# Performance work log

Measured on AMD Instinct MI355X. Metric: run time of the kernel, lower is better.

Reference implementation:

```python
import jax, jax.numpy as jnp
import numpy as np

N, E, G = 50000, 500000, 64
F_IN, H, C = 10, 4, 64
HC = H * C  # 256
NCLS = 8
BN_EPS = 1e-5


def _bn(x, g, b, m, v):
    # eval-mode BatchNorm1d with running stats
    return (x - m) * jax.lax.rsqrt(v + BN_EPS) * g + b


def _gat(x, src, dst, W, a_s, a_d, b):
    # PyG GATConv (concat=True): h=[N,H,C]; e_ij=leakyrelu(a_s.h_j + a_d.h_i);
    # softmax over incoming edges of each destination node; scatter-add.
    n = x.shape[0]
    h = (x @ W).reshape(n, H, C)
    es = jnp.einsum('nhc,hc->nh', h, a_s)  # source term per node
    ed = jnp.einsum('nhc,hc->nh', h, a_d)  # dest term per node
    e = jax.nn.leaky_relu(es[src] + ed[dst], 0.2)            # [E2,H]
    m = jax.ops.segment_max(e, dst, num_segments=n)
    ex = jnp.exp(e - m[dst])
    s = jax.ops.segment_sum(ex, dst, num_segments=n)
    alpha = ex / (s[dst] + 1e-16)                             # [E2,H]
    out = jax.ops.segment_sum(h[src] * alpha[:, :, None], dst, num_segments=n)
    return out.reshape(n, HC) + b, alpha


def _gcn(x, src, dst, W, b):
    n = x.shape[0]
    deg = jax.ops.segment_sum(jnp.ones_like(src, dtype=x.dtype), dst, num_segments=n)
    dinv = jax.lax.rsqrt(jnp.maximum(deg, 1.0))
    norm = dinv[src] * dinv[dst]
    xw = x @ W
    return jax.ops.segment_sum(xw[src] * norm[:, None], dst, num_segments=n) + b


def setup_inputs() -> dict:
    key = jax.random.key(0)
    ks = jax.random.split(key, 48)
    r = lambda i, sh, sc=0.1: jax.random.normal(ks[i], sh, dtype=jnp.float32) * sc
    p = {}
    p['x'] = jax.random.normal(ks[0], (N, F_IN), dtype=jnp.float32)
    p['edge_index'] = jax.random.randint(ks[1], (2, E), 0, N, dtype=jnp.int32)
    p['batch'] = jnp.sort(jax.random.randint(ks[2], (N,), 0, G, dtype=jnp.int32))
    # GAT1
    p['W1'] = r(3, (F_IN, HC)); p['as1'] = r(4, (H, C)); p['ad1'] = r(5, (H, C)); p['bi1'] = r(6, (HC,))
    # GAT2
    p['W2'] = r(7, (HC, HC)); p['as2'] = r(8, (H, C)); p['ad2'] = r(9, (H, C)); p['bi2'] = r(10, (HC,))
    # BN running stats / affine
    for i, (nm, d) in enumerate([('bn1', HC), ('bn2', HC), ('bn3', C)]):
        k0 = 11 + 4 * i
        p[nm + '_g'] = 1.0 + r(k0, (d,))
        p[nm + '_b'] = r(k0 + 1, (d,))
        p[nm + '_m'] = r(k0 + 2, (d,))
        p[nm + '_v'] = 1.0 + jax.random.uniform(ks[k0 + 3], (d,), dtype=jnp.float32) * 0.5
    # GCN
    p['Wg'] = r(23, (HC, C)); p['bg'] = r(24, (C,))
    # reduce_dim
    p['Wr'] = r(25, (2 * C, C)); p['br'] = r(26, (C,))
    # rul head
    p['Wh1'] = r(27, (C, 32)); p['bh1'] = r(28, (32,))
    p['Wh2'] = r(29, (32, 16)); p['bh2'] = r(30, (16,))
    p['Wh3'] = r(31, (16, 1)); p['bh3'] = r(32, (1,))
    # location head
    p['Wl1'] = r(33, (C, 32)); p['bl1'] = r(34, (32,))
    p['Wl2'] = r(35, (32, NCLS)); p['bl2'] = r(36, (NCLS,))
    # energy head
    p['We1'] = r(37, (C, 16)); p['be1'] = r(38, (16,))
    p['We2'] = r(39, (16, 1)); p['be2'] = r(40, (1,))
    return p


def reference(x, edge_index, batch,
              W1, as1, ad1, bi1, W2, as2, ad2, bi2,
              bn1_g, bn1_b, bn1_m, bn1_v, bn2_g, bn2_b, bn2_m, bn2_v,
              bn3_g, bn3_b, bn3_m, bn3_v,
              Wg, bg, Wr, br,
              Wh1, bh1, Wh2, bh2, Wh3, bh3,
              Wl1, bl1, Wl2, bl2, We1, be1, We2, be2):
    n = x.shape[0]
    loop = jnp.arange(n, dtype=edge_index.dtype)
    src = jnp.concatenate([edge_index[0], loop])
    dst = jnp.concatenate([edge_index[1], loop])

    h, alpha1 = _gat(x, src, dst, W1, as1, ad1, bi1)
    h = jax.nn.elu(_bn(h, bn1_g, bn1_b, bn1_m, bn1_v))  # dropout = identity (eval)
    h, alpha2 = _gat(h, src, dst, W2, as2, ad2, bi2)
    h = jax.nn.elu(_bn(h, bn2_g, bn2_b, bn2_m, bn2_v))
    h = _gcn(h, src, dst, Wg, bg)
    h = jax.nn.elu(_bn(h, bn3_g, bn3_b, bn3_m, bn3_v))  # node embeddings [N,64]

    cnt = jax.ops.segment_sum(jnp.ones((n,), h.dtype), batch, num_segments=G)
    x_mean = jax.ops.segment_sum(h, batch, num_segments=G) / jnp.maximum(cnt, 1.0)[:, None]
    x_max = jax.ops.segment_max(h, batch, num_segments=G)
    x_max = jnp.where(cnt[:, None] > 0, x_max, 0.0)
    xg = jnp.concatenate([x_mean, x_max], axis=1) @ Wr + br  # [G,64]

    t = jax.nn.relu(xg @ Wh1 + bh1)
    t = jax.nn.relu(t @ Wh2 + bh2)
    rul = jax.nn.sigmoid(t @ Wh3 + bh3) * 100.0
    loc = jax.nn.relu(xg @ Wl1 + bl1) @ Wl2 + bl2
    en = jax.nn.relu(xg @ We1 + be1) @ We2 + be2
    return rul, loc, en, h, xg
```

## Files before the change

kernel.cpp:

```cpp
#include <hip/hip_runtime.h>
#include <math.h>

#define SCAN_BLK 1024
#define BN_EPS 1e-5f

typedef __attribute__((ext_vector_type(8))) short short8;
typedef __attribute__((ext_vector_type(4))) short short4v;
typedef __attribute__((ext_vector_type(4))) float f32x4;

__device__ __forceinline__ float eluf(float x){ return x > 0.f ? x : (expf(x) - 1.f); }
__device__ __forceinline__ unsigned short f2bf(float f){
  unsigned u = __float_as_uint(f);
  u += 0x7FFFu + ((u >> 16) & 1u);
  return (unsigned short)(u >> 16);
}
__device__ __forceinline__ float bf2f(unsigned short s){
  return __uint_as_float(((unsigned)s) << 16);
}
__device__ __forceinline__ unsigned fmap(float f){
  unsigned b = __float_as_uint(f);
  return (b & 0x80000000u) ? ~b : (b | 0x80000000u);
}
__device__ __forceinline__ float funmap(unsigned u){
  unsigned b = (u & 0x80000000u) ? (u ^ 0x80000000u) : ~u;
  return __uint_as_float(b);
}
__device__ __forceinline__ float lrelu(float a){ return a > 0.f ? a : 0.2f * a; }

__global__ void k_count(const int* __restrict__ ei, int* __restrict__ deg, int ne, int e2)
{
  int t = blockIdx.x * 256 + threadIdx.x;
  if (t >= e2) return;
  int dst = (t < ne) ? ei[ne + t] : t - ne;
  atomicAdd(&deg[dst], 1);
}

__global__ void k_scan1(const int* __restrict__ deg, int* __restrict__ rowptr,
                        int* __restrict__ partials, int n)
{
  __shared__ int sh[SCAN_BLK];
  int t = threadIdx.x, base = blockIdx.x * SCAN_BLK;
  int v = (base + t < n) ? deg[base + t] : 0;
  sh[t] = v;
  __syncthreads();
  for (int off = 1; off < SCAN_BLK; off <<= 1) {
    int u = 0;
    if (t >= off) u = sh[t - off];
    __syncthreads();
    if (t >= off) sh[t] += u;
    __syncthreads();
  }
  if (base + t < n) rowptr[base + t] = sh[t] - v;
  if (t == SCAN_BLK - 1) partials[blockIdx.x] = sh[t];
}

__global__ void k_scan2(int* __restrict__ rowptr, const int* __restrict__ partials, int n)
{
  int base = blockIdx.x * SCAN_BLK;
  int add = 0;
  for (int i = 0; i < blockIdx.x; i++) add += partials[i];
  int t = threadIdx.x;
  if (base + t < n) rowptr[base + t] += add;
}

__global__ void k_fill(const int* __restrict__ ei, const int* __restrict__ rowptr,
                       int* __restrict__ cursor, int* __restrict__ col, int ne, int e2)
{
  int t = blockIdx.x * 256 + threadIdx.x;
  if (t >= e2) return;
  int src, dst;
  if (t < ne) { src = ei[t]; dst = ei[ne + t]; } else { src = dst = t - ne; }
  int pos = rowptr[dst] + atomicAdd(&cursor[dst], 1);
  col[pos] = src;
}

__global__ void k_dinv(const int* __restrict__ deg, float* __restrict__ dinv, int n)
{
  int t = blockIdx.x * 256 + threadIdx.x;
  if (t < n) dinv[t] = rsqrtf(fmaxf((float)deg[t], 1.f));
}

__global__ void k_pack(const float* __restrict__ W, unsigned short* __restrict__ Wp,
                       int N, int nct)
{
  int tid = threadIdx.x;
  int l = tid >> 3, j = tid & 7;
  int ct = blockIdx.x >> 3, ks = blockIdx.x & 7;
  int k = ks * 32 + (l >> 4) * 8 + j;
  int c = ct * 16 + (l & 15);
  Wp[(size_t)(ks * nct + ct) * 512 + tid] = f2bf(W[(size_t)k * N + c]);
}

__global__ void k_pack_es(const float* __restrict__ WasT, unsigned short* __restrict__ Wes)
{
  int tid = threadIdx.x;
  int l = tid >> 3, j = tid & 7;
  int ks = blockIdx.x;
  int k = ks * 32 + (l >> 4) * 8 + j;
  int c = l & 15;
  float v = (c < 8) ? WasT[(size_t)c * 256 + k] : 0.f;
  Wes[(size_t)(ks * 64 + l) * 8 + j] = f2bf(v);
}

__global__ void k_prep1(const float* __restrict__ W1, const float* __restrict__ as1,
                        const float* __restrict__ ad1,
                        float* __restrict__ Ws1, float* __restrict__ Wd1)
{
  int t = threadIdx.x;
  if (t >= 80) return;
  int half = t / 40, r = t % 40;
  int k = r / 4, h = r % 4;
  const float* a = half ? ad1 : as1;
  float s = 0.f;
  for (int c = 0; c < 64; c++) s += W1[k * 256 + h * 64 + c] * a[h * 64 + c];
  (half ? Wd1 : Ws1)[k * 4 + h] = s;
}

__global__ void k_prep2(const float* __restrict__ W2, const float* __restrict__ as2,
                        const float* __restrict__ ad2, float* __restrict__ WasT)
{
  int g = blockIdx.x * 256 + threadIdx.x;
  if (g >= 2048) return;
  int half = g >= 1024, r = g & 1023;
  int i = r >> 2, h = r & 3;
  const float* a = half ? ad2 : as2;
  float s = 0.f;
  for (int c = 0; c < 64; c++) s += W2[(size_t)i * 256 + h * 64 + c] * a[h * 64 + c];
  WasT[(size_t)(half * 4 + h) * 256 + i] = s;
}

__global__ void k_prep_bn(const float* __restrict__ bi1, const float* __restrict__ g1,
                          const float* __restrict__ b1, const float* __restrict__ m1,
                          const float* __restrict__ v1,
                          const float* __restrict__ bi2, const float* __restrict__ g2,
                          const float* __restrict__ b2, const float* __restrict__ m2,
                          const float* __restrict__ v2,
                          float* __restrict__ A1, float* __restrict__ B1,
                          float* __restrict__ A2, float* __restrict__ B2)
{
  int c = threadIdx.x;
  if (c < 256) {
    float a = rsqrtf(v1[c] + BN_EPS) * g1[c];
    A1[c] = a; B1[c] = (bi1[c] - m1[c]) * a + b1[c];
    a = rsqrtf(v2[c] + BN_EPS) * g2[c];
    A2[c] = a; B2[c] = (bi2[c] - m2[c]) * a + b2[c];
  }
}

__global__ void k_es1(const float* __restrict__ x, const float* __restrict__ Ws1,
                      const float* __restrict__ Wd1,
                      float* __restrict__ es, float* __restrict__ ed, int n)
{
  int t = blockIdx.x * 256 + threadIdx.x;
  if (t >= n) return;
  float xr[10];
  #pragma unroll
  for (int k = 0; k < 10; k++) xr[k] = x[(size_t)t * 10 + k];
  float e0[4] = {0,0,0,0}, e1[4] = {0,0,0,0};
  #pragma unroll
  for (int k = 0; k < 10; k++) {
    #pragma unroll
    for (int h = 0; h < 4; h++) {
      e0[h] += xr[k] * Ws1[k * 4 + h];
      e1[h] += xr[k] * Wd1[k * 4 + h];
    }
  }
  *(float4*)&es[t * 4] = make_float4(e0[0], e0[1], e0[2], e0[3]);
  *(float4*)&ed[t * 4] = make_float4(e1[0], e1[1], e1[2], e1[3]);
}

__global__ __launch_bounds__(256) void k_mfma_esed(
    const unsigned short* __restrict__ act, const unsigned short* __restrict__ Wes,
    float* __restrict__ es, float* __restrict__ ed, int n)
{
  int tid = threadIdx.x, wave = tid >> 6, lane = tid & 63;
  int l15 = lane & 15, lg = lane >> 4;
  int rbase = blockIdx.x * 64 + wave * 16;
  int arow = rbase + l15; if (arow > n - 1) arow = n - 1;
  const unsigned short* ap = &act[(size_t)arow * 256 + lg * 8];

  f32x4 acc = {0.f, 0.f, 0.f, 0.f};
  #pragma unroll
  for (int ks = 0; ks < 8; ks++) {
    short8 a = *(const short8*)(ap + ks * 32);
    short8 b = *(const short8*)&Wes[(size_t)(ks * 64 + lane) * 8];
    acc = __builtin_amdgcn_mfma_f32_16x16x32_bf16(a, b, acc, 0, 0, 0);
  }

  #pragma unroll
  for (int r = 0; r < 4; r++) {
    int row = rbase + lg * 4 + r;
    if (row < n) {
      if (l15 < 4)            es[row * 4 + l15] = acc[r];
      else if (l15 < 8)       ed[row * 4 + (l15 - 4)] = acc[r];
    }
  }
}

__global__ void k_xagg(const int* __restrict__ rowptr, const int* __restrict__ deg,
                       const int* __restrict__ col,
                       const float* __restrict__ es, const float* __restrict__ ed,
                       const float* __restrict__ x, float* __restrict__ xa, int n)
{
  int d = blockIdx.x * 4 + (threadIdx.x >> 6);
  if (d >= n) return;
  int lane = threadIdx.x & 63;
  int slot = lane >> 4, k = lane & 15;
  int start = rowptr[d], cnt = deg[d];
  bool active = (k < 10);
  float4 edv = *(const float4*)&ed[d * 4];

  float a0 = 0.f, a1 = 0.f, a2 = 0.f, a3 = 0.f;
  float s0 = 0.f, s1 = 0.f, s2 = 0.f, s3 = 0.f;
  int i = slot;
  for (; i + 4 < cnt; i += 8) {
    int e0 = start + i, e1 = start + i + 4;
    int sa = col[e0], sb = col[e1];
    float4 u0 = *(const float4*)&es[sa * 4];
    float4 u1 = *(const float4*)&es[sb * 4];
    float x0 = active ? x[(size_t)sa * 10 + k] : 0.f;
    float x1 = active ? x[(size_t)sb * 10 + k] : 0.f;
    float ex;
    ex = expf(lrelu(u0.x + edv.x)); a0 += ex * x0; s0 += ex;
    ex = expf(lrelu(u0.y + edv.y)); a1 += ex * x0; s1 += ex;
    ex = expf(lrelu(u0.z + edv.z)); a2 += ex * x0; s2 += ex;
    ex = expf(lrelu(u0.w + edv.w)); a3 += ex * x0; s3 += ex;
    ex = expf(lrelu(u1.x + edv.x)); a0 += ex * x1; s0 += ex;
    ex = expf(lrelu(u1.y + edv.y)); a1 += ex * x1; s1 += ex;
    ex = expf(lrelu(u1.z + edv.z)); a2 += ex * x1; s2 += ex;
    ex = expf(lrelu(u1.w + edv.w)); a3 += ex * x1; s3 += ex;
  }
  if (i < cnt) {
    int e0 = start + i;
    int sa = col[e0];
    float4 u0 = *(const float4*)&es[sa * 4];
    float x0 = active ? x[(size_t)sa * 10 + k] : 0.f;
    float ex;
    ex = expf(lrelu(u0.x + edv.x)); a0 += ex * x0; s0 += ex;
    ex = expf(lrelu(u0.y + edv.y)); a1 += ex * x0; s1 += ex;
    ex = expf(lrelu(u0.z + edv.z)); a2 += ex * x0; s2 += ex;
    ex = expf(lrelu(u0.w + edv.w)); a3 += ex * x0; s3 += ex;
  }
  a0 += __shfl_xor(a0, 16, 64); a0 += __shfl_xor(a0, 32, 64);
  a1 += __shfl_xor(a1, 16, 64); a1 += __shfl_xor(a1, 32, 64);
  a2 += __shfl_xor(a2, 16, 64); a2 += __shfl_xor(a2, 32, 64);
  a3 += __shfl_xor(a3, 16, 64); a3 += __shfl_xor(a3, 32, 64);
  s0 += __shfl_xor(s0, 16, 64); s0 += __shfl_xor(s0, 32, 64);
  s1 += __shfl_xor(s1, 16, 64); s1 += __shfl_xor(s1, 32, 64);
  s2 += __shfl_xor(s2, 16, 64); s2 += __shfl_xor(s2, 32, 64);
  s3 += __shfl_xor(s3, 16, 64); s3 += __shfl_xor(s3, 32, 64);

  if (slot == 0 && active) {
    float* xo = &xa[(size_t)d * 40];
    xo[k]      = a0 / (s0 + 1e-16f);
    xo[10 + k] = a1 / (s1 + 1e-16f);
    xo[20 + k] = a2 / (s2 + 1e-16f);
    xo[30 + k] = a3 / (s3 + 1e-16f);
  }
}

__global__ void k_gemm_xa(const float* __restrict__ xa, const float* __restrict__ W1,
                          const float* __restrict__ A1, const float* __restrict__ B1,
                          unsigned short* __restrict__ actA, int n)
{
  __shared__ float xal[160];
  int tid = threadIdx.x;
  int n0 = blockIdx.x * 4;
  if (tid < 160 && (size_t)n0 * 40 + tid < (size_t)n * 40)
    xal[tid] = xa[(size_t)n0 * 40 + tid];
  __syncthreads();
  int c = tid, h = c >> 6;
  float w[10];
  #pragma unroll
  for (int k = 0; k < 10; k++) w[k] = W1[k * 256 + c];
  float a1 = A1[c], b1 = B1[c];
  #pragma unroll
  for (int m = 0; m < 4; m++) {
    int nn = n0 + m;
    if (nn >= n) break;
    float acc = 0.f;
    #pragma unroll
    for (int k = 0; k < 10; k++) acc += xal[m * 40 + h * 10 + k] * w[k];
    actA[(size_t)nn * 256 + c] = f2bf(eluf(acc * a1 + b1));
  }
}

__global__ void k_gat_gather(const int* __restrict__ rowptr, const int* __restrict__ deg,
                             const int* __restrict__ col,
                             const float* __restrict__ es, const float* __restrict__ ed,
                             const unsigned short* __restrict__ act,
                             unsigned short* __restrict__ outb, int n)
{
  int d = blockIdx.x * 4 + (threadIdx.x >> 6);
  if (d >= n) return;
  int lane = threadIdx.x & 63;
  int half = lane >> 5, l32 = lane & 31;
  int c8 = l32 * 8, head = l32 >> 3;
  int start = rowptr[d], cnt = deg[d];
  float edh = ed[d * 4 + head];

  float acc[8] = {0.f,0.f,0.f,0.f,0.f,0.f,0.f,0.f};
  float sex = 0.f;
  int T = (cnt > half) ? ((cnt - half + 1) >> 1) : 0;
  int ebase = start + half;
  int t = 0;
  for (; t + 4 <= T; t += 4) {
    int e0 = ebase + 2 * t, e1 = e0 + 2, e2 = e0 + 4, e3 = e0 + 6;
    int s0 = col[e0], s1 = col[e1], s2 = col[e2], s3 = col[e3];
    float x0 = expf(lrelu(es[s0 * 4 + head] + edh));
    float x1 = expf(lrelu(es[s1 * 4 + head] + edh));
    float x2 = expf(lrelu(es[s2 * 4 + head] + edh));
    float x3 = expf(lrelu(es[s3 * 4 + head] + edh));
    short8 h0 = *(const short8*)&act[(size_t)s0 * 256 + c8];
    short8 h1 = *(const short8*)&act[(size_t)s1 * 256 + c8];
    short8 h2 = *(const short8*)&act[(size_t)s2 * 256 + c8];
    short8 h3 = *(const short8*)&act[(size_t)s3 * 256 + c8];
    #pragma unroll
    for (int j = 0; j < 8; j++) {
      acc[j] += bf2f((unsigned short)h0[j]) * x0 + bf2f((unsigned short)h1[j]) * x1
              + bf2f((unsigned short)h2[j]) * x2 + bf2f((unsigned short)h3[j]) * x3;
    }
    sex += x0 + x1 + x2 + x3;
  }
  for (; t < T; t++) {
    int e0 = ebase + 2 * t;
    int s0 = col[e0];
    float x0 = expf(lrelu(es[s0 * 4 + head] + edh));
    short8 h0 = *(const short8*)&act[(size_t)s0 * 256 + c8];
    #pragma unroll
    for (int j = 0; j < 8; j++) acc[j] += bf2f((unsigned short)h0[j]) * x0;
    sex += x0;
  }
  #pragma unroll
  for (int j = 0; j < 8; j++)
    acc[j] += __shfl_xor(acc[j], 32, 64);
  sex += __shfl_xor(sex, 32, 64);

  if (half == 0) {
    float sv = 1.f / (sex + 1e-16f);
    short8 o;
    #pragma unroll
    for (int j = 0; j < 8; j++) o[j] = (short)f2bf(acc[j] * sv);
    *(short8*)&outb[(size_t)d * 256 + c8] = o;
  }
}

template<int NCT, bool BNEPI>
__global__ __launch_bounds__(256) void k_mfma_gemm(
    const unsigned short* __restrict__ act, const unsigned short* __restrict__ Wp,
    unsigned short* __restrict__ outb,
    const float* __restrict__ Abn, const float* __restrict__ Bbn, int n)
{
  __shared__ unsigned short bsh[NCT * 512];
  int tid = threadIdx.x, wave = tid >> 6, lane = tid & 63;
  int l15 = lane & 15, lg = lane >> 4;
  int rbase = blockIdx.x * 64 + wave * 16;
  int arow = rbase + l15; if (arow > n - 1) arow = n - 1;
  const unsigned short* ap = &act[(size_t)arow * 256 + lg * 8];

  constexpr int NCH = (NCT >= 4) ? NCT / 4 : 1;
  f32x4 acc[NCT];
  f32x4 z = {0.f, 0.f, 0.f, 0.f};
  #pragma unroll
  for (int ct = 0; ct < NCT; ct++) acc[ct] = z;

  for (int ks = 0; ks < 8; ks++) {
    const unsigned short* src = Wp + (size_t)ks * NCT * 512 + wave * NCT * 128;
    short8 stg[NCH];
    #pragma unroll
    for (int c = 0; c < NCH; c++)
      stg[c] = *(const short8*)(src + c * 512 + lane * 8);
    short8 a = *(const short8*)(ap + ks * 32);
    __syncthreads();
    #pragma unroll
    for (int c = 0; c < NCH; c++)
      *(short8*)&bsh[wave * NCT * 128 + c * 512 + lane * 8] = stg[c];
    __syncthreads();
    #pragma unroll
    for (int ct = 0; ct < NCT; ct++) {
      short8 b = *(const short8*)&bsh[(ct * 64 + lane) * 8];
      acc[ct] = __builtin_amdgcn_mfma_f32_16x16x32_bf16(a, b, acc[ct], 0, 0, 0);
    }
  }

  float abn[NCT], bbn[NCT];
  if (BNEPI) {
    #pragma unroll
    for (int ct = 0; ct < NCT; ct++) {
      abn[ct] = Abn[ct * 16 + l15];
      bbn[ct] = Bbn[ct * 16 + l15];
    }
  }
  #pragma unroll
  for (int r = 0; r < 4; r++) {
    int row = rbase + lg * 4 + r;
    if (row < n) {
      #pragma unroll
      for (int ct = 0; ct < NCT; ct++) {
        float v = acc[ct][r];
        if (BNEPI) v = eluf(v * abn[ct] + bbn[ct]);
        outb[(size_t)row * (NCT * 16) + ct * 16 + l15] = f2bf(v);
      }
    }
  }
}

__global__ void k_gcn_gather(const int* __restrict__ rowptr, const int* __restrict__ deg,
                             const int* __restrict__ col, const float* __restrict__ dinv,
                             const unsigned short* __restrict__ xwb,
                             const float* __restrict__ bias,
                             const float* __restrict__ gg, const float* __restrict__ bb,
                             const float* __restrict__ mm, const float* __restrict__ vv,
                             float* __restrict__ hout, int n)
{
  int d = blockIdx.x * 4 + (threadIdx.x >> 6);
  if (d >= n) return;
  int lane = threadIdx.x & 63;
  int slot = lane >> 3, cg = (lane & 7) * 8;
  int start = rowptr[d], cnt = deg[d];
  float dinvd = rsqrtf(fmaxf((float)cnt, 1.f));

  float acc[8] = {0.f,0.f,0.f,0.f,0.f,0.f,0.f,0.f};
  int i = slot;
  for (; i + 8 < cnt; i += 16) {
    int s0 = col[start + i], s1 = col[start + i + 8];
    float n0 = dinv[s0], n1 = dinv[s1];
    short8 h0 = *(const short8*)&xwb[(size_t)s0 * 64 + cg];
    short8 h1 = *(const short8*)&xwb[(size_t)s1 * 64 + cg];
    #pragma unroll
    for (int j = 0; j < 8; j++)
      acc[j] += bf2f((unsigned short)h0[j]) * n0 + bf2f((unsigned short)h1[j]) * n1;
  }
  if (i < cnt) {
    int s0 = col[start + i];
    float n0 = dinv[s0];
    short8 h0 = *(const short8*)&xwb[(size_t)s0 * 64 + cg];
    #pragma unroll
    for (int j = 0; j < 8; j++)
      acc[j] += bf2f((unsigned short)h0[j]) * n0;
  }
  #pragma unroll
  for (int j = 0; j < 8; j++) {
    acc[j] += __shfl_xor(acc[j], 8, 64);
    acc[j] += __shfl_xor(acc[j], 16, 64);
    acc[j] += __shfl_xor(acc[j], 32, 64);
    acc[j] *= dinvd;
  }

  if (lane < 8) {
    float out[8];
    #pragma unroll
    for (int j = 0; j < 8; j++) {
      int c = cg + j;
      float r = ((acc[j] + bias[c]) - mm[c]) * rsqrtf(vv[c] + BN_EPS) * gg[c] + bb[c];
      out[j] = eluf(r);
    }
    *(float4*)&hout[(size_t)d * 64 + cg]     = make_float4(out[0], out[1], out[2], out[3]);
    *(float4*)&hout[(size_t)d * 64 + cg + 4] = make_float4(out[4], out[5], out[6], out[7]);
  }
}

__global__ void k_pool_partial(const float* __restrict__ hout, const int* __restrict__ batch,
                               float* __restrict__ psum, unsigned* __restrict__ pmaxu,
                               int n)
{
  int wave = threadIdx.x >> 6, lane = threadIdx.x & 63;
  int wbase = blockIdx.x * 128 + wave * 32;
  int wend = wbase + 32; if (wend > n) wend = n;
  if (wbase >= n) return;

  int g_cur = -1;
  float s = 0.f, mx = -1e30f;
  for (int node = wbase; node < wend; node++) {
    int g = batch[node];
    if (g != g_cur) {
      if (g_cur >= 0) {
        atomicAdd(&psum[g_cur * 64 + lane], s);
        atomicMax(&pmaxu[g_cur * 64 + lane], fmap(mx));
      }
      g_cur = g; s = 0.f; mx = -1e30f;
    }
    float v = hout[(size_t)node * 64 + lane];
    s += v;
    mx = fmaxf(mx, v);
  }
  if (g_cur >= 0) {
    atomicAdd(&psum[g_cur * 64 + lane], s);
    atomicMax(&pmaxu[g_cur * 64 + lane], fmap(mx));
  }
}

__global__ void k_heads(const float* __restrict__ psum, const unsigned* __restrict__ pmaxu,
                        const int* __restrict__ batch,
                        const float* __restrict__ Wr, const float* __restrict__ br,
                        const float* __restrict__ Wh1, const float* __restrict__ bh1,
                        const float* __restrict__ Wh2, const float* __restrict__ bh2,
                        const float* __restrict__ Wh3, const float* __restrict__ bh3,
                        const float* __restrict__ Wl1, const float* __restrict__ bl1,
                        const float* __restrict__ Wl2, const float* __restrict__ bl2,
                        const float* __restrict__ We1, const float* __restrict__ be1,
                        const float* __restrict__ We2, const float* __restrict__ be2,
                        float* __restrict__ outp, int n, int xg_off)
{
  __shared__ float cat[128], xg[64], t1[32], t2[16], l1[32], e1[16];
  int g = blockIdx.x, c = threadIdx.x;

  int lo = 0, hi = n;
  while (lo < hi) { int mid = (lo + hi) >> 1; if (batch[mid] < g) lo = mid + 1; else hi = mid; }
  int start = lo;
  lo = start; hi = n;
  while (lo < hi) { int mid = (lo + hi) >> 1; if (batch[mid] < g + 1) lo = mid + 1; else hi = mid; }
  int cntg = lo - start;

  float mean = psum[g * 64 + c] / fmaxf((float)cntg, 1.f);
  float mxv = (cntg > 0) ? funmap(pmaxu[g * 64 + c]) : 0.f;
  cat[c] = mean; cat[64 + c] = mxv;
  __syncthreads();
  float a = br[c];
  for (int i = 0; i < 128; i++) a += cat[i] * Wr[i * 64 + c];
  xg[c] = a;
  outp[xg_off + g * 64 + c] = a;
  __syncthreads();
  if (c < 32) {
    float u = bh1[c]; for (int i = 0; i < 64; i++) u += xg[i] * Wh1[i * 32 + c];
    t1[c] = fmaxf(u, 0.f);
    float v = bl1[c]; for (int i = 0; i < 64; i++) v += xg[i] * Wl1[i * 32 + c];
    l1[c] = fmaxf(v, 0.f);
  }
  __syncthreads();
  if (c < 16) {
    float u = bh2[c]; for (int i = 0; i < 32; i++) u += t1[i] * Wh2[i * 16 + c];
    t2[c] = fmaxf(u, 0.f);
    float v = be1[c]; for (int i = 0; i < 64; i++) v += xg[i] * We1[i * 16 + c];
    e1[c] = fmaxf(v, 0.f);
  }
  __syncthreads();
  if (c < 8) {
    float v = bl2[c]; for (int i = 0; i < 32; i++) v += l1[i] * Wl2[i * 8 + c];
    outp[64 + g * 8 + c] = v;
  }
  if (c == 0) {
    float u = bh3[0]; for (int i = 0; i < 16; i++) u += t2[i] * Wh3[i];
    outp[g] = 100.f / (1.f + expf(-u));
    float v = be2[0]; for (int i = 0; i < 16; i++) v += e1[i] * We2[i];
    outp[576 + g] = v;
  }
}

extern "C" void kernel_launch(void* const* d_in, const int* in_sizes, int n_in,
                              void* d_out, int out_size, void* d_ws, size_t ws_size,
                              hipStream_t stream)
{
  const float* x    = (const float*)d_in[0];
  const int*   ei   = (const int*)d_in[1];
  const int*   batch= (const int*)d_in[2];
  const float* W1   = (const float*)d_in[3];
  const float* as1  = (const float*)d_in[4];
  const float* ad1  = (const float*)d_in[5];
  const float* bi1  = (const float*)d_in[6];
  const float* W2   = (const float*)d_in[7];
  const float* as2  = (const float*)d_in[8];
  const float* ad2  = (const float*)d_in[9];
  const float* bi2  = (const float*)d_in[10];
  const float* bn1g = (const float*)d_in[11];
  const float* bn1b = (const float*)d_in[12];
  const float* bn1m = (const float*)d_in[13];
  const float* bn1v = (const float*)d_in[14];
  const float* bn2g = (const float*)d_in[15];
  const float* bn2b = (const float*)d_in[16];
  const float* bn2m = (const float*)d_in[17];
  const float* bn2v = (const float*)d_in[18];
  const float* bn3g = (const float*)d_in[19];
  const float* bn3b = (const float*)d_in[20];
  const float* bn3m = (const float*)d_in[21];
  const float* bn3v = (const float*)d_in[22];
  const float* Wg   = (const float*)d_in[23];
  const float* bg   = (const float*)d_in[24];
  const float* Wr   = (const float*)d_in[25];
  const float* br   = (const float*)d_in[26];
  const float* Wh1  = (const float*)d_in[27];
  const float* bh1  = (const float*)d_in[28];
  const float* Wh2  = (const float*)d_in[29];
  const float* bh2  = (const float*)d_in[30];
  const float* Wh3  = (const float*)d_in[31];
  const float* bh3  = (const float*)d_in[32];
  const float* Wl1  = (const float*)d_in[33];
  const float* bl1  = (const float*)d_in[34];
  const float* Wl2  = (const float*)d_in[35];
  const float* bl2  = (const float*)d_in[36];
  const float* We1  = (const float*)d_in[37];
  const float* be1  = (const float*)d_in[38];
  const float* We2  = (const float*)d_in[39];
  const float* be2  = (const float*)d_in[40];

  const int n  = in_sizes[2];
  const int ne = in_sizes[1] / 2;
  const int e2 = ne + n;

  float* ws = (float*)d_ws;
  size_t off = 0;
  unsigned short* bufA = (unsigned short*)(ws + off); off += (size_t)n * 128;
  unsigned short* bufB = (unsigned short*)(ws + off); off += (size_t)n * 128;
  float* xa   = ws + off; off += (size_t)n * 40;
  float* es   = ws + off; off += (size_t)n * 4;
  float* ed   = ws + off; off += (size_t)n * 4;
  float* dinv = ws + off; off += (size_t)n;
  int* rowptr = (int*)(ws + off); off += (size_t)n + 1;
  int* deg    = (int*)(ws + off); off += (size_t)n;
  int* cursor = (int*)(ws + off); off += (size_t)n;
  int* col    = (int*)(ws + off); off += (size_t)e2;
  int* partials = (int*)(ws + off); off += 64;
  unsigned short* Wp2 = (unsigned short*)(ws + off); off += 32768;
  unsigned short* Wpg = (unsigned short*)(ws + off); off += 8192;
  unsigned short* Wes = (unsigned short*)(ws + off); off += 2048;
  float* Ws1  = ws + off; off += 40;
  float* Wd1  = ws + off; off += 40;
  float* WasT = ws + off; off += 2048;
  float* A1   = ws + off; off += 256;
  float* B1   = ws + off; off += 256;
  float* A2   = ws + off; off += 256;
  float* B2   = ws + off; off += 256;
  float* psum = ws + off; off += 64 * 64;
  unsigned* pmaxu = (unsigned*)(ws + off); off += 64 * 64;

  unsigned short* actA = bufA;
  unsigned short* agg2 = bufB;
  unsigned short* actB = bufA;
  unsigned short* xwb  = bufB;

  float* outp = (float*)d_out;
  float* hout = outp + 640;
  const int xg_off = 640 + n * 64;

  const int eb   = (e2 + 255) / 256;
  const int gb1  = (n + 3) / 4;
  const int gmb  = (n + 63) / 64;
  const int nsb  = (n + SCAN_BLK - 1) / SCAN_BLK;

  hipMemsetAsync(deg, 0, (size_t)n * sizeof(int), stream);
  hipMemsetAsync(cursor, 0, (size_t)n * sizeof(int), stream);
  k_count<<<eb, 256, 0, stream>>>(ei, deg, ne, e2);
  k_scan1<<<nsb, SCAN_BLK, 0, stream>>>(deg, rowptr, partials, n);
  k_scan2<<<nsb, SCAN_BLK, 0, stream>>>(rowptr, partials, n);
  k_fill<<<eb, 256, 0, stream>>>(ei, rowptr, cursor, col, ne, e2);
  k_dinv<<<(n + 255) / 256, 256, 0, stream>>>(deg, dinv, n);
  k_pack<<<128, 512, 0, stream>>>(W2, Wp2, 256, 16);
  k_pack<<<32, 512, 0, stream>>>(Wg, Wpg, 64, 4);
  k_prep1<<<1, 128, 0, stream>>>(W1, as1, ad1, Ws1, Wd1);
  k_prep2<<<8, 256, 0, stream>>>(W2, as2, ad2, WasT);
  k_pack_es<<<8, 512, 0, stream>>>(WasT, Wes);
  k_prep_bn<<<1, 256, 0, stream>>>(bi1, bn1g, bn1b, bn1m, bn1v,
                                   bi2, bn2g, bn2b, bn2m, bn2v,
                                   A1, B1, A2, B2);

  k_es1<<<(n + 255) / 256, 256, 0, stream>>>(x, Ws1, Wd1, es, ed, n);
  k_xagg<<<gb1, 256, 0, stream>>>(rowptr, deg, col, es, ed, x, xa, n);
  k_gemm_xa<<<gb1, 256, 0, stream>>>(xa, W1, A1, B1, actA, n);

  k_mfma_esed<<<gmb, 256, 0, stream>>>(actA, Wes, es, ed, n);
  k_gat_gather<<<gb1, 256, 0, stream>>>(rowptr, deg, col, es, ed, actA, agg2, n);
  k_mfma_gemm<16, true><<<gmb, 256, 0, stream>>>(agg2, Wp2, actB, A2, B2, n);

  k_mfma_gemm<4, false><<<gmb, 256, 0, stream>>>(actB, Wpg, xwb, nullptr, nullptr, n);
  k_gcn_gather<<<gb1, 256, 0, stream>>>(rowptr, deg, col, dinv, xwb,
                                        bg, bn3g, bn3b, bn3m, bn3v, hout, n);

  hipMemsetAsync(psum, 0, 64 * 64 * sizeof(float), stream);
  hipMemsetAsync(pmaxu, 0, 64 * 64 * sizeof(unsigned), stream);
  k_pool_partial<<<(n + 127) / 128, 256, 0, stream>>>(hout, batch, psum, pmaxu, n);
  k_heads<<<64, 64, 0, stream>>>(psum, pmaxu, batch, Wr, br,
                                 Wh1, bh1, Wh2, bh2, Wh3, bh3,
                                 Wl1, bl1, Wl2, bl2, We1, be1, We2, be2,
                                 outp, n, xg_off);
}
```

Baseline: 296.8 us.

## Slice GAT1 activations into channel-major 32-wide planes for cache-local gathers

The first-layer activations are stored as eight planes of 32 channels each ([slice][node][32]) instead of row-major 256-wide rows. The GAT2 gather kernel now runs one block group per slice, so each slice pass only touches a 3.2 MB plane that fits better in L2/MALL. The ES/ED MFMA kernel reads from the sliced layout. In exchange, every edge's col and es values are reloaded and the exp is recomputed once per slice, which is eight times the index and exp work.

```diff
diff --git a/kernel.cpp b/kernel.cpp
--- a/kernel.cpp
+++ b/kernel.cpp
@@ -170,19 +170,18 @@
 }
 
 __global__ __launch_bounds__(256) void k_mfma_esed(
-    const unsigned short* __restrict__ act, const unsigned short* __restrict__ Wes,
+    const unsigned short* __restrict__ actAs, const unsigned short* __restrict__ Wes,
     float* __restrict__ es, float* __restrict__ ed, int n)
 {
   int tid = threadIdx.x, wave = tid >> 6, lane = tid & 63;
   int l15 = lane & 15, lg = lane >> 4;
   int rbase = blockIdx.x * 64 + wave * 16;
   int arow = rbase + l15; if (arow > n - 1) arow = n - 1;
-  const unsigned short* ap = &act[(size_t)arow * 256 + lg * 8];
 
   f32x4 acc = {0.f, 0.f, 0.f, 0.f};
   #pragma unroll
   for (int ks = 0; ks < 8; ks++) {
-    short8 a = *(const short8*)(ap + ks * 32);
+    short8 a = *(const short8*)&actAs[(size_t)ks * n * 32 + (size_t)arow * 32 + lg * 8];
     short8 b = *(const short8*)&Wes[(size_t)(ks * 64 + lane) * 8];
     acc = __builtin_amdgcn_mfma_f32_16x16x32_bf16(a, b, acc, 0, 0, 0);
   }
@@ -261,7 +260,7 @@
 
 __global__ void k_gemm_xa(const float* __restrict__ xa, const float* __restrict__ W1,
                           const float* __restrict__ A1, const float* __restrict__ B1,
-                          unsigned short* __restrict__ actA, int n)
+                          unsigned short* __restrict__ actAs, int n)
 {
   __shared__ float xal[160];
   int tid = threadIdx.x;
@@ -270,6 +269,7 @@
     xal[tid] = xa[(size_t)n0 * 40 + tid];
   __syncthreads();
   int c = tid, h = c >> 6;
+  int slice = c >> 5, cin = c & 31;
   float w[10];
   #pragma unroll
   for (int k = 0; k < 10; k++) w[k] = W1[k * 256 + c];
@@ -281,68 +281,57 @@
     float acc = 0.f;
     #pragma unroll
     for (int k = 0; k < 10; k++) acc += xal[m * 40 + h * 10 + k] * w[k];
-    actA[(size_t)nn * 256 + c] = f2bf(eluf(acc * a1 + b1));
+    actAs[(size_t)slice * n * 32 + (size_t)nn * 32 + cin] = f2bf(eluf(acc * a1 + b1));
   }
 }
 
 __global__ void k_gat_gather(const int* __restrict__ rowptr, const int* __restrict__ deg,
                              const int* __restrict__ col,
                              const float* __restrict__ es, const float* __restrict__ ed,
-                             const unsigned short* __restrict__ act,
+                             const unsigned short* __restrict__ actAs,
                              unsigned short* __restrict__ outb, int n)
 {
-  int d = blockIdx.x * 4 + (threadIdx.x >> 6);
+  int slice = blockIdx.x & 7, grp = blockIdx.x >> 3;
+  int wave = threadIdx.x >> 6, lane = threadIdx.x & 63;
+  int slot = lane >> 3, c4 = (lane & 7) * 4;
+  int d = grp * 32 + wave * 8 + slot;
   if (d >= n) return;
-  int lane = threadIdx.x & 63;
-  int half = lane >> 5, l32 = lane & 31;
-  int c8 = l32 * 8, head = l32 >> 3;
+  int head = slice >> 1;
   int start = rowptr[d], cnt = deg[d];
   float edh = ed[d * 4 + head];
-
-  float acc[8] = {0.f,0.f,0.f,0.f,0.f,0.f,0.f,0.f};
-  float sex = 0.f;
-  int T = (cnt > half) ? ((cnt - half + 1) >> 1) : 0;
-  int ebase = start + half;
-  int t = 0;
-  for (; t + 4 <= T; t += 4) {
-    int e0 = ebase + 2 * t, e1 = e0 + 2, e2 = e0 + 4, e3 = e0 + 6;
-    int s0 = col[e0], s1 = col[e1], s2 = col[e2], s3 = col[e3];
+  const unsigned short* base = actAs + (size_t)slice * n * 32;
+
+  float a0 = 0.f, a1 = 0.f, a2 = 0.f, a3 = 0.f, sex = 0.f;
+  int i = 0;
+  for (; i + 2 <= cnt; i += 2) {
+    int s0 = col[start + i], s1 = col[start + i + 1];
     float x0 = expf(lrelu(es[s0 * 4 + head] + edh));
     float x1 = expf(lrelu(es[s1 * 4 + head] + edh));
-    float x2 = expf(lrelu(es[s2 * 4 + head] + edh));
-    float x3 = expf(lrelu(es[s3 * 4 + head] + edh));
-    short8 h0 = *(const short8*)&act[(size_t)s0 * 256 + c8];
-    short8 h1 = *(const short8*)&act[(size_t)s1 * 256 + c8];
-    short8 h2 = *(const short8*)&act[(size_t)s2 * 256 + c8];
-    short8 h3 = *(const short8*)&act[(size_t)s3 * 256 + c8];
-    #pragma unroll
-    for (int j = 0; j < 8; j++) {
-      acc[j] += bf2f((unsigned short)h0[j]) * x0 + bf2f((unsigned short)h1[j]) * x1
-              + bf2f((unsigned short)h2[j]) * x2 + bf2f((unsigned short)h3[j]) * x3;
-    }
-    sex += x0 + x1 + x2 + x3;
-  }
-  for (; t < T; t++) {
-    int e0 = ebase + 2 * t;
-    int s0 = col[e0];
+    short4v h0 = *(const short4v*)&base[(size_t)s0 * 32 + c4];
+    short4v h1 = *(const short4v*)&base[(size_t)s1 * 32 + c4];
+    a0 += bf2f((unsigned short)h0[0]) * x0 + bf2f((unsigned short)h1[0]) * x1;
+    a1 += bf2f((unsigned short)h0[1]) * x0 + bf2f((unsigned short)h1[1]) * x1;
+    a2 += bf2f((unsigned short)h0[2]) * x0 + bf2f((unsigned short)h1[2]) * x1;
+    a3 += bf2f((unsigned short)h0[3]) * x0 + bf2f((unsigned short)h1[3]) * x1;
+    sex += x0 + x1;
+  }
+  if (i < cnt) {
+    int s0 = col[start + i];
     float x0 = expf(lrelu(es[s0 * 4 + head] + edh));
-    short8 h0 = *(const short8*)&act[(size_t)s0 * 256 + c8];
-    #pragma unroll
-    for (int j = 0; j < 8; j++) acc[j] += bf2f((unsigned short)h0[j]) * x0;
+    short4v h0 = *(const short4v*)&base[(size_t)s0 * 32 + c4];
+    a0 += bf2f((unsigned short)h0[0]) * x0;
+    a1 += bf2f((unsigned short)h0[1]) * x0;
+    a2 += bf2f((unsigned short)h0[2]) * x0;
+    a3 += bf2f((unsigned short)h0[3]) * x0;
     sex += x0;
   }
-  #pragma unroll
-  for (int j = 0; j < 8; j++)
-    acc[j] += __shfl_xor(acc[j], 32, 64);
-  sex += __shfl_xor(sex, 32, 64);
-
-  if (half == 0) {
-    float sv = 1.f / (sex + 1e-16f);
-    short8 o;
-    #pragma unroll
-    for (int j = 0; j < 8; j++) o[j] = (short)f2bf(acc[j] * sv);
-    *(short8*)&outb[(size_t)d * 256 + c8] = o;
-  }
+  float sv = 1.f / (sex + 1e-16f);
+  short4v o;
+  o[0] = (short)f2bf(a0 * sv);
+  o[1] = (short)f2bf(a1 * sv);
+  o[2] = (short)f2bf(a2 * sv);
+  o[3] = (short)f2bf(a3 * sv);
+  *(short4v*)&outb[(size_t)d * 256 + slice * 32 + c4] = o;
 }
 
 template<int NCT, bool BNEPI>
@@ -623,10 +612,10 @@
   float* psum = ws + off; off += 64 * 64;
   unsigned* pmaxu = (unsigned*)(ws + off); off += 64 * 64;
 
-  unsigned short* actA = bufA;
-  unsigned short* agg2 = bufB;
-  unsigned short* actB = bufA;
-  unsigned short* xwb  = bufB;
+  unsigned short* actAs = bufA;
+  unsigned short* agg2  = bufB;
+  unsigned short* actB  = bufA;
+  unsigned short* xwb   = bufB;
 
   float* outp = (float*)d_out;
   float* hout = outp + 640;
@@ -636,6 +625,7 @@
   const int gb1  = (n + 3) / 4;
   const int gmb  = (n + 63) / 64;
   const int nsb  = (n + SCAN_BLK - 1) / SCAN_BLK;
+  const int gsl  = 8 * ((n + 31) / 32);
 
   hipMemsetAsync(deg, 0, (size_t)n * sizeof(int), stream);
   hipMemsetAsync(cursor, 0, (size_t)n * sizeof(int), stream);
@@ -655,10 +645,10 @@
 
   k_es1<<<(n + 255) / 256, 256, 0, stream>>>(x, Ws1, Wd1, es, ed, n);
   k_xagg<<<gb1, 256, 0, stream>>>(rowptr, deg, col, es, ed, x, xa, n);
-  k_gemm_xa<<<gb1, 256, 0, stream>>>(xa, W1, A1, B1, actA, n);
-
-  k_mfma_esed<<<gmb, 256, 0, stream>>>(actA, Wes, es, ed, n);
-  k_gat_gather<<<gb1, 256, 0, stream>>>(rowptr, deg, col, es, ed, actA, agg2, n);
+  k_gemm_xa<<<gb1, 256, 0, stream>>>(xa, W1, A1, B1, actAs, n);
+
+  k_mfma_esed<<<gmb, 256, 0, stream>>>(actAs, Wes, es, ed, n);
+  k_gat_gather<<<gsl, 256, 0, stream>>>(rowptr, deg, col, es, ed, actAs, agg2, n);
   k_mfma_gemm<16, true><<<gmb, 256, 0, stream>>>(agg2, Wp2, actB, A2, B2, n);
 
   k_mfma_gemm<4, false><<<gmb, 256, 0, stream>>>(actB, Wpg, xwb, nullptr, nullptr, n);
```

Result: slower. 318.5 us (+7.3%).

## Fuse GAT2 and GCN GEMMs, fold attention scores and prep kernels, merge memsets

Applied to the files above, without the earlier changes.

Merges the GAT2 GEMM with its BN/ELU epilogue and the GCN projection GEMM into one kernel. The activated tile stays in LDS in bf16 and feeds the second MFMA directly, so the intermediate activation never round-trips through global memory. Layer-2 attention scores are computed inside the layer-1 feature kernel with a wave reduction, which drops a separate MFMA pass over actA. dinv is folded into the scan, the prep kernels are merged, and adjacent memsets are combined to cut launch count. The trade-off is higher LDS use per block (about 50KB), which may lower occupancy, and a switch from bf16 to fp32 math for es/ed.

```diff
diff --git a/kernel.cpp b/kernel.cpp
--- a/kernel.cpp
+++ b/kernel.cpp
@@ -36,7 +36,7 @@
 }
 
 __global__ void k_scan1(const int* __restrict__ deg, int* __restrict__ rowptr,
-                        int* __restrict__ partials, int n)
+                        int* __restrict__ partials, float* __restrict__ dinv, int n)
 {
   __shared__ int sh[SCAN_BLK];
   int t = threadIdx.x, base = blockIdx.x * SCAN_BLK;
@@ -50,7 +50,10 @@
     if (t >= off) sh[t] += u;
     __syncthreads();
   }
-  if (base + t < n) rowptr[base + t] = sh[t] - v;
+  if (base + t < n) {
+    rowptr[base + t] = sh[t] - v;
+    dinv[base + t] = rsqrtf(fmaxf((float)v, 1.f));
+  }
   if (t == SCAN_BLK - 1) partials[blockIdx.x] = sh[t];
 }
 
@@ -74,12 +77,6 @@
   col[pos] = src;
 }
 
-__global__ void k_dinv(const int* __restrict__ deg, float* __restrict__ dinv, int n)
-{
-  int t = blockIdx.x * 256 + threadIdx.x;
-  if (t < n) dinv[t] = rsqrtf(fmaxf((float)deg[t], 1.f));
-}
-
 __global__ void k_pack(const float* __restrict__ W, unsigned short* __restrict__ Wp,
                        int N, int nct)
 {
@@ -91,59 +88,45 @@
   Wp[(size_t)(ks * nct + ct) * 512 + tid] = f2bf(W[(size_t)k * N + c]);
 }
 
-__global__ void k_pack_es(const float* __restrict__ WasT, unsigned short* __restrict__ Wes)
-{
-  int tid = threadIdx.x;
-  int l = tid >> 3, j = tid & 7;
-  int ks = blockIdx.x;
-  int k = ks * 32 + (l >> 4) * 8 + j;
-  int c = l & 15;
-  float v = (c < 8) ? WasT[(size_t)c * 256 + k] : 0.f;
-  Wes[(size_t)(ks * 64 + l) * 8 + j] = f2bf(v);
-}
-
-__global__ void k_prep1(const float* __restrict__ W1, const float* __restrict__ as1,
-                        const float* __restrict__ ad1,
-                        float* __restrict__ Ws1, float* __restrict__ Wd1)
+__global__ void k_prep_all(const float* __restrict__ W1, const float* __restrict__ as1,
+                           const float* __restrict__ ad1,
+                           const float* __restrict__ W2, const float* __restrict__ as2,
+                           const float* __restrict__ ad2,
+                           const float* __restrict__ bi1, const float* __restrict__ g1,
+                           const float* __restrict__ b1, const float* __restrict__ m1,
+                           const float* __restrict__ v1,
+                           const float* __restrict__ bi2, const float* __restrict__ g2,
+                           const float* __restrict__ b2, const float* __restrict__ m2,
+                           const float* __restrict__ v2,
+                           float* __restrict__ Ws1, float* __restrict__ Wd1,
+                           float* __restrict__ WasT,
+                           float* __restrict__ A1, float* __restrict__ B1,
+                           float* __restrict__ A2, float* __restrict__ B2)
 {
   int t = threadIdx.x;
-  if (t >= 80) return;
-  int half = t / 40, r = t % 40;
-  int k = r / 4, h = r % 4;
-  const float* a = half ? ad1 : as1;
-  float s = 0.f;
-  for (int c = 0; c < 64; c++) s += W1[k * 256 + h * 64 + c] * a[h * 64 + c];
-  (half ? Wd1 : Ws1)[k * 4 + h] = s;
-}
-
-__global__ void k_prep2(const float* __restrict__ W2, const float* __restrict__ as2,
-                        const float* __restrict__ ad2, float* __restrict__ WasT)
-{
-  int g = blockIdx.x * 256 + threadIdx.x;
-  if (g >= 2048) return;
-  int half = g >= 1024, r = g & 1023;
-  int i = r >> 2, h = r & 3;
-  const float* a = half ? ad2 : as2;
-  float s = 0.f;
-  for (int c = 0; c < 64; c++) s += W2[(size_t)i * 256 + h * 64 + c] * a[h * 64 + c];
-  WasT[(size_t)(half * 4 + h) * 256 + i] = s;
-}
-
-__global__ void k_prep_bn(const float* __restrict__ bi1, const float* __restrict__ g1,
-                          const float* __restrict__ b1, const float* __restrict__ m1,
-                          const float* __restrict__ v1,
-                          const float* __restrict__ bi2, const float* __restrict__ g2,
-                          const float* __restrict__ b2, const float* __restrict__ m2,
-                          const float* __restrict__ v2,
-                          float* __restrict__ A1, float* __restrict__ B1,
-                          float* __restrict__ A2, float* __restrict__ B2)
-{
-  int c = threadIdx.x;
-  if (c < 256) {
-    float a = rsqrtf(v1[c] + BN_EPS) * g1[c];
-    A1[c] = a; B1[c] = (bi1[c] - m1[c]) * a + b1[c];
-    a = rsqrtf(v2[c] + BN_EPS) * g2[c];
-    A2[c] = a; B2[c] = (bi2[c] - m2[c]) * a + b2[c];
+  if (blockIdx.x < 8) {
+    int g = blockIdx.x * 256 + t;
+    int half = g >= 1024, r = g & 1023;
+    int i = r >> 2, h = r & 3;
+    const float* a = half ? ad2 : as2;
+    float s = 0.f;
+    for (int c = 0; c < 64; c++) s += W2[(size_t)i * 256 + h * 64 + c] * a[h * 64 + c];
+    WasT[(size_t)(half * 4 + h) * 256 + i] = s;
+  } else {
+    if (t < 80) {
+      int half = t / 40, r = t % 40;
+      int k = r / 4, h = r % 4;
+      const float* a = half ? ad1 : as1;
+      float s = 0.f;
+      for (int c = 0; c < 64; c++) s += W1[k * 256 + h * 64 + c] * a[h * 64 + c];
+      (half ? Wd1 : Ws1)[k * 4 + h] = s;
+    }
+    if (t < 256) {
+      float a = rsqrtf(v1[t] + BN_EPS) * g1[t];
+      A1[t] = a; B1[t] = (bi1[t] - m1[t]) * a + b1[t];
+      a = rsqrtf(v2[t] + BN_EPS) * g2[t];
+      A2[t] = a; B2[t] = (bi2[t] - m2[t]) * a + b2[t];
+    }
   }
 }
 
@@ -167,34 +150,6 @@
   }
   *(float4*)&es[t * 4] = make_float4(e0[0], e0[1], e0[2], e0[3]);
   *(float4*)&ed[t * 4] = make_float4(e1[0], e1[1], e1[2], e1[3]);
-}
-
-__global__ __launch_bounds__(256) void k_mfma_esed(
-    const unsigned short* __restrict__ act, const unsigned short* __restrict__ Wes,
-    float* __restrict__ es, float* __restrict__ ed, int n)
-{
-  int tid = threadIdx.x, wave = tid >> 6, lane = tid & 63;
-  int l15 = lane & 15, lg = lane >> 4;
-  int rbase = blockIdx.x * 64 + wave * 16;
-  int arow = rbase + l15; if (arow > n - 1) arow = n - 1;
-  const unsigned short* ap = &act[(size_t)arow * 256 + lg * 8];
-
-  f32x4 acc = {0.f, 0.f, 0.f, 0.f};
-  #pragma unroll
-  for (int ks = 0; ks < 8; ks++) {
-    short8 a = *(const short8*)(ap + ks * 32);
-    short8 b = *(const short8*)&Wes[(size_t)(ks * 64 + lane) * 8];
-    acc = __builtin_amdgcn_mfma_f32_16x16x32_bf16(a, b, acc, 0, 0, 0);
-  }
-
-  #pragma unroll
-  for (int r = 0; r < 4; r++) {
-    int row = rbase + lg * 4 + r;
-    if (row < n) {
-      if (l15 < 4)            es[row * 4 + l15] = acc[r];
-      else if (l15 < 8)       ed[row * 4 + (l15 - 4)] = acc[r];
-    }
-  }
 }
 
 __global__ void k_xagg(const int* __restrict__ rowptr, const int* __restrict__ deg,
@@ -261,9 +216,12 @@
 
 __global__ void k_gemm_xa(const float* __restrict__ xa, const float* __restrict__ W1,
                           const float* __restrict__ A1, const float* __restrict__ B1,
-                          unsigned short* __restrict__ actA, int n)
+                          const float* __restrict__ WasT,
+                          unsigned short* __restrict__ actA,
+                          float* __restrict__ es, float* __restrict__ ed, int n)
 {
   __shared__ float xal[160];
+  __shared__ float actl[4][256];
   int tid = threadIdx.x;
   int n0 = blockIdx.x * 4;
   if (tid < 160 && (size_t)n0 * 40 + tid < (size_t)n * 40)
@@ -281,7 +239,31 @@
     float acc = 0.f;
     #pragma unroll
     for (int k = 0; k < 10; k++) acc += xal[m * 40 + h * 10 + k] * w[k];
-    actA[(size_t)nn * 256 + c] = f2bf(eluf(acc * a1 + b1));
+    float v = eluf(acc * a1 + b1);
+    actl[m][c] = v;
+    actA[(size_t)nn * 256 + c] = f2bf(v);
+  }
+  __syncthreads();
+  int wave = tid >> 6, lane = tid & 63;
+  int nn = n0 + wave;
+  if (nn < n) {
+    float e[8] = {0,0,0,0,0,0,0,0};
+    int c0 = lane * 4;
+    #pragma unroll
+    for (int j = 0; j < 4; j++) {
+      float av = actl[wave][c0 + j];
+      #pragma unroll
+      for (int q = 0; q < 8; q++) e[q] += av * WasT[q * 256 + c0 + j];
+    }
+    #pragma unroll
+    for (int off = 1; off < 64; off <<= 1) {
+      #pragma unroll
+      for (int q = 0; q < 8; q++) e[q] += __shfl_xor(e[q], off, 64);
+    }
+    if (lane == 0) {
+      *(float4*)&es[nn * 4] = make_float4(e[0], e[1], e[2], e[3]);
+      *(float4*)&ed[nn * 4] = make_float4(e[4], e[5], e[6], e[7]);
+    }
   }
 }
 
@@ -345,50 +327,75 @@
   }
 }
 
-template<int NCT, bool BNEPI>
-__global__ __launch_bounds__(256) void k_mfma_gemm(
-    const unsigned short* __restrict__ act, const unsigned short* __restrict__ Wp,
-    unsigned short* __restrict__ outb,
-    const float* __restrict__ Abn, const float* __restrict__ Bbn, int n)
-{
-  __shared__ unsigned short bsh[NCT * 512];
+__global__ __launch_bounds__(256) void k_mfma_gemm2(
+    const unsigned short* __restrict__ agg2, const unsigned short* __restrict__ Wp2,
+    const unsigned short* __restrict__ Wpg,
+    const float* __restrict__ Abn, const float* __restrict__ Bbn,
+    unsigned short* __restrict__ xwb, int n)
+{
+  __shared__ unsigned short bsh[16 * 512];
+  __shared__ unsigned short act2[64 * 264];
   int tid = threadIdx.x, wave = tid >> 6, lane = tid & 63;
   int l15 = lane & 15, lg = lane >> 4;
   int rbase = blockIdx.x * 64 + wave * 16;
   int arow = rbase + l15; if (arow > n - 1) arow = n - 1;
-  const unsigned short* ap = &act[(size_t)arow * 256 + lg * 8];
-
-  constexpr int NCH = (NCT >= 4) ? NCT / 4 : 1;
-  f32x4 acc[NCT];
+  const unsigned short* ap = &agg2[(size_t)arow * 256 + lg * 8];
+
+  f32x4 acc[16];
   f32x4 z = {0.f, 0.f, 0.f, 0.f};
   #pragma unroll
-  for (int ct = 0; ct < NCT; ct++) acc[ct] = z;
+  for (int ct = 0; ct < 16; ct++) acc[ct] = z;
 
   for (int ks = 0; ks < 8; ks++) {
-    const unsigned short* src = Wp + (size_t)ks * NCT * 512 + wave * NCT * 128;
-    short8 stg[NCH];
-    #pragma unroll
-    for (int c = 0; c < NCH; c++)
+    const unsigned short* src = Wp2 + (size_t)ks * 16 * 512 + wave * 16 * 128;
+    short8 stg[4];
+    #pragma unroll
+    for (int c = 0; c < 4; c++)
       stg[c] = *(const short8*)(src + c * 512 + lane * 8);
     short8 a = *(const short8*)(ap + ks * 32);
     __syncthreads();
     #pragma unroll
-    for (int c = 0; c < NCH; c++)
-      *(short8*)&bsh[wave * NCT * 128 + c * 512 + lane * 8] = stg[c];
+    for (int c = 0; c < 4; c++)
+      *(short8*)&bsh[wave * 16 * 128 + c * 512 + lane * 8] = stg[c];
     __syncthreads();
     #pragma unroll
-    for (int ct = 0; ct < NCT; ct++) {
+    for (int ct = 0; ct < 16; ct++) {
       short8 b = *(const short8*)&bsh[(ct * 64 + lane) * 8];
       acc[ct] = __builtin_amdgcn_mfma_f32_16x16x32_bf16(a, b, acc[ct], 0, 0, 0);
     }
   }
 
-  float abn[NCT], bbn[NCT];
-  if (BNEPI) {
-    #pragma unroll
-    for (int ct = 0; ct < NCT; ct++) {
-      abn[ct] = Abn[ct * 16 + l15];
-      bbn[ct] = Bbn[ct * 16 + l15];
+  float abn[16], bbn[16];
+  #pragma unroll
+  for (int ct = 0; ct < 16; ct++) {
+    abn[ct] = Abn[ct * 16 + l15];
+    bbn[ct] = Bbn[ct * 16 + l15];
+  }
+  #pragma unroll
+  for (int r = 0; r < 4; r++) {
+    int row = rbase + lg * 4 + r;
+    if (row < n) {
+      int rl = wave * 16 + lg * 4 + r;
+      #pragma unroll
+      for (int ct = 0; ct < 16; ct++) {
+        float v = eluf(acc[r < 0 ? 0 : ct][r] * abn[ct] + bbn[ct]);
+        act2[rl * 264 + ct * 16 + l15] = f2bf(v);
+      }
+    }
+  }
+  __syncthreads();
+
+  f32x4 acc2[4];
+  #pragma unroll
+  for (int ct = 0; ct < 4; ct++) acc2[ct] = z;
+  const unsigned short* a2p = &act2[(wave * 16 + l15) * 264];
+  #pragma unroll
+  for (int ks = 0; ks < 8; ks++) {
+    short8 a2 = *(const short8*)(a2p + ks * 32 + lg * 8);
+    #pragma unroll
+    for (int ct = 0; ct < 4; ct++) {
+      short8 b = *(const short8*)&Wpg[(size_t)(ks * 4 + ct) * 512 + lane * 8];
+      acc2[ct] = __builtin_amdgcn_mfma_f32_16x16x32_bf16(a2, b, acc2[ct], 0, 0, 0);
     }
   }
   #pragma unroll
@@ -396,11 +403,8 @@
     int row = rbase + lg * 4 + r;
     if (row < n) {
       #pragma unroll
-      for (int ct = 0; ct < NCT; ct++) {
-        float v = acc[ct][r];
-        if (BNEPI) v = eluf(v * abn[ct] + bbn[ct]);
-        outb[(size_t)row * (NCT * 16) + ct * 16 + l15] = f2bf(v);
-      }
+      for (int ct = 0; ct < 4; ct++)
+        xwb[(size_t)row * 64 + ct * 16 + l15] = f2bf(acc2[ct][r]);
     }
   }
 }
@@ -612,7 +616,6 @@
   int* partials = (int*)(ws + off); off += 64;
   unsigned short* Wp2 = (unsigned short*)(ws + off); off += 32768;
   unsigned short* Wpg = (unsigned short*)(ws + off); off += 8192;
-  unsigned short* Wes = (unsigned short*)(ws + off); off += 2048;
   float* Ws1  = ws + off; off += 40;
   float* Wd1  = ws + off; off += 40;
   float* WasT = ws + off; off += 2048;
@@ -625,8 +628,7 @@
 
   unsigned short* actA = bufA;
   unsigned short* agg2 = bufB;
-  unsigned short* actB = bufA;
-  unsigned short* xwb  = bufB;
+  unsigned short* xwb  = bufA;
 
   float* outp = (float*)d_out;
   float* hout = outp + 640;
@@ -637,36 +639,29 @@
   const int gmb  = (n + 63) / 64;
   const int nsb  = (n + SCAN_BLK - 1) / SCAN_BLK;
 
-  hipMemsetAsync(deg, 0, (size_t)n * sizeof(int), stream);
-  hipMemsetAsync(cursor, 0, (size_t)n * sizeof(int), stream);
+  hipMemsetAsync(deg, 0, (size_t)2 * n * sizeof(int), stream);
   k_count<<<eb, 256, 0, stream>>>(ei, deg, ne, e2);
-  k_scan1<<<nsb, SCAN_BLK, 0, stream>>>(deg, rowptr, partials, n);
+  k_scan1<<<nsb, SCAN_BLK, 0, stream>>>(deg, rowptr, partials, dinv, n);
   k_scan2<<<nsb, SCAN_BLK, 0, stream>>>(rowptr, partials, n);
   k_fill<<<eb, 256, 0, stream>>>(ei, rowptr, cursor, col, ne, e2);
-  k_dinv<<<(n + 255) / 256, 256, 0, stream>>>(deg, dinv, n);
   k_pack<<<128, 512, 0, stream>>>(W2, Wp2, 256, 16);
   k_pack<<<32, 512, 0, stream>>>(Wg, Wpg, 64, 4);
-  k_prep1<<<1, 128, 0, stream>>>(W1, as1, ad1, Ws1, Wd1);
-  k_prep2<<<8, 256, 0, stream>>>(W2, as2, ad2, WasT);
-  k_pack_es<<<8, 512, 0, stream>>>(WasT, Wes);
-  k_prep_bn<<<1, 256, 0, stream>>>(bi1, bn1g, bn1b, bn1m, bn1v,
-                                   bi2, bn2g, bn2b, bn2m, bn2v,
-                                   A1, B1, A2, B2);
+  k_prep_all<<<9, 256, 0, stream>>>(W1, as1, ad1, W2, as2, ad2,
+                                    bi1, bn1g, bn1b, bn1m, bn1v,
+                                    bi2, bn2g, bn2b, bn2m, bn2v,
+                                    Ws1, Wd1, WasT, A1, B1, A2, B2);
 
   k_es1<<<(n + 255) / 256, 256, 0, stream>>>(x, Ws1, Wd1, es, ed, n);
   k_xagg<<<gb1, 256, 0, stream>>>(rowptr, deg, col, es, ed, x, xa, n);
-  k_gemm_xa<<<gb1, 256, 0, stream>>>(xa, W1, A1, B1, actA, n);
-
-  k_mfma_esed<<<gmb, 256, 0, stream>>>(actA, Wes, es, ed, n);
+  k_gemm_xa<<<gb1, 256, 0, stream>>>(xa, W1, A1, B1, WasT, actA, es, ed, n);
+
   k_gat_gather<<<gb1, 256, 0, stream>>>(rowptr, deg, col, es, ed, actA, agg2, n);
-  k_mfma_gemm<16, true><<<gmb, 256, 0, stream>>>(agg2, Wp2, actB, A2, B2, n);
-
-  k_mfma_gemm<4, false><<<gmb, 256, 0, stream>>>(actB, Wpg, xwb, nullptr, nullptr, n);
+  k_mfma_gemm2<<<gmb, 256, 0, stream>>>(agg2, Wp2, Wpg, A2, B2, xwb, n);
+
   k_gcn_gather<<<gb1, 256, 0, stream>>>(rowptr, deg, col, dinv, xwb,
                                         bg, bn3g, bn3b, bn3m, bn3v, hout, n);
 
-  hipMemsetAsync(psum, 0, 64 * 64 * sizeof(float), stream);
-  hipMemsetAsync(pmaxu, 0, 64 * 64 * sizeof(unsigned), stream);
+  hipMemsetAsync(psum, 0, 2 * 64 * 64 * sizeof(float), stream);
   k_pool_partial<<<(n + 127) / 128, 256, 0, stream>>>(hout, batch, psum, pmaxu, n);
   k_heads<<<64, 64, 0, stream>>>(psum, pmaxu, batch, Wr, br,
                                  Wh1, bh1, Wh2, bh2, Wh3, bh3,
```

New measurement: 288.0 us. -3.0%, faster.
